# Performance work log

Hardware: AMD Instinct MI355X
Metric: run time of the kernel (lower is better)

The kernel has to match this reference:

```python
import jax, jax.numpy as jnp
import numpy as np

T, B, F, L = 512, 4096, 16, 4  # seq_len, batch, input_size, n_layers; hidden_size H = 1


def _lstm_layer(seq, W_ih, W_hh, b_ih, b_hh):
    """Single unidirectional LSTM layer, H=1.
    seq: [T, B, in]; W_ih: [4, in]; W_hh: [4, 1]; b_ih, b_hh: [4].
    Returns (hs [T,B,1], h_T [B,1], c_T [B,1]). Gate order i,f,g,o (PyTorch).
    """
    # Input contribution for all timesteps at once (the only sizeable GEMM).
    gx = jnp.einsum('tbi,gi->tbg', seq, W_ih) + b_ih + b_hh  # [T, B, 4]
    Bb = seq.shape[1]
    h0 = jnp.zeros((Bb, 1), seq.dtype)
    c0 = jnp.zeros((Bb, 1), seq.dtype)

    def step(carry, g):
        h, c = carry
        gates = g + h @ W_hh.T  # [B, 4]
        i = jax.nn.sigmoid(gates[:, 0:1])
        f = jax.nn.sigmoid(gates[:, 1:2])
        gg = jnp.tanh(gates[:, 2:3])
        o = jax.nn.sigmoid(gates[:, 3:4])
        c = f * c + i * gg
        h = o * jnp.tanh(c)
        return (h, c), h

    (hT, cT), hs = jax.lax.scan(step, (h0, c0), gx)
    return hs, hT, cT


def setup_inputs() -> dict:
    key = jax.random.key(0)
    ks = jax.random.split(key, 6)
    s = 0.5  # ~U(-1,1) stdev scale; 1/sqrt(H)=1 in torch init
    return {
        'x': jax.random.normal(ks[0], (T, B, F), jnp.float32),
        'W_ih0': jax.random.normal(ks[1], (4, F), jnp.float32) * s,
        'W_ih_rest': jax.random.normal(ks[2], (L - 1, 4, 1), jnp.float32) * s,
        'W_hh': jax.random.normal(ks[3], (L, 4, 1), jnp.float32) * s,
        'b_ih': jax.random.normal(ks[4], (L, 4), jnp.float32) * s,
        'b_hh': jax.random.normal(ks[5], (L, 4), jnp.float32) * s,
    }


def reference(x, W_ih0, W_ih_rest, W_hh, b_ih, b_hh):
    seq = x
    hns, cns = [], []
    for l in range(L):
        W_ih_l = W_ih0 if l == 0 else W_ih_rest[l - 1]
        seq, hT, cT = _lstm_layer(seq, W_ih_l, W_hh[l], b_ih[l], b_hh[l])
        hns.append(hT)
        cns.append(cT)
    output = seq                      # [T, B, 1] last-layer hidden sequence
    hn = jnp.stack(hns, axis=0)       # [L, B, 1]
    cn = jnp.stack(cns, axis=0)       # [L, B, 1]
    return output, hn, cn
```

## Files before the change

kernel.cpp:

```cpp
#include <hip/hip_runtime.h>

#define T_DIM 512
#define B_DIM 4096
#define L_DIM 4
#define LOG2E 1.44269504088896f

typedef float f4 __attribute__((ext_vector_type(4)));

template <int CTRL>
__device__ __forceinline__ float dpp_mov(float v) {
  int r = __builtin_amdgcn_update_dpp(0, __builtin_bit_cast(int, v), CTRL, 0xf, 0xf, true);
  return __builtin_bit_cast(float, r);
}
template <int CTRL>
__device__ __forceinline__ float qp_add(float v) { return v + dpp_mov<CTRL>(v); }

__global__ __launch_bounds__(256, 1) void lstm_fused(
    const float* __restrict__ x,
    const float* __restrict__ Wih0,
    const float* __restrict__ Wrest,
    const float* __restrict__ Whh,
    const float* __restrict__ bih, const float* __restrict__ bhh,
    float* __restrict__ out) {
  const int tid = threadIdx.x;
  const int lane = tid & 63;
  const int wid = tid >> 6;
  const int g = lane & 3;
  const int l = (lane >> 2) & 3;
  const int c = (lane >> 4) & 3;
  const int chain = blockIdx.x * 16 + wid * 4 + c;
  const bool l0 = (l == 0);

  auto sg = [](int i) { return (i == 2) ? 2.0f * LOG2E : -LOG2E; };

  const float whh  = sg(g) * Whh[l * 4 + g];
  const float wih  = l0 ? 0.f : sg(g) * Wrest[(l - 1) * 4 + g];
  const float base = l0 ? 0.f : sg(g) * (bih[l * 4 + g] + bhh[l * 4 + g]);
  f4 wx;
  {
    const f4 wv = ((const f4*)Wih0)[g * 4 + l];
    const float s = sg(g);
    wx.x = s * wv.x; wx.y = s * wv.y; wx.z = s * wv.z; wx.w = s * wv.w;
  }
  const float dinit = l0 ? sg(g) * (bih[g] + bhh[g]) : 0.f;
  const float vm = (g == 2) ? -2.f : 1.f;
  const float va = (g == 2) ? 1.f : 0.f;

  const f4* __restrict__ xp = (const f4*)x;
  const size_t xoff = (size_t)chain * 4 + (size_t)l;
  float* __restrict__ po = out + chain;

  float h = 0.f, cs = 0.f;
  f4 A[8], B[8];

#define LOAD8(R, t0)                                                        \
  do {                                                                      \
    R[0] = xp[(size_t)((t0) + 0) * 16384 + xoff];                           \
    R[1] = xp[(size_t)((t0) + 1) * 16384 + xoff];                           \
    R[2] = xp[(size_t)((t0) + 2) * 16384 + xoff];                           \
    R[3] = xp[(size_t)((t0) + 3) * 16384 + xoff];                           \
    R[4] = xp[(size_t)((t0) + 4) * 16384 + xoff];                           \
    R[5] = xp[(size_t)((t0) + 5) * 16384 + xoff];                           \
    R[6] = xp[(size_t)((t0) + 6) * 16384 + xoff];                           \
    R[7] = xp[(size_t)((t0) + 7) * 16384 + xoff];                           \
  } while (0)

  auto dotD = [&](f4 xv) -> float {
    float p = fmaf(xv.x, wx.x, fmaf(xv.y, wx.y, fmaf(xv.z, wx.z, fmaf(xv.w, wx.w, dinit))));
    p = qp_add<0x124>(p);
    p = qp_add<0x128>(p);
    return p;
  };

  auto cellv = [&](int k, float D, bool guard) {
    float hin = dpp_mov<0x114>(h);
    float pb = l0 ? D : base;
    float gate = fmaf(whh, h, fmaf(wih, hin, pb));

    float r = __builtin_amdgcn_rcpf(1.0f + __builtin_amdgcn_exp2f(gate));
    float v = fmaf(vm, r, va);

    float i_ = dpp_mov<0x00>(v);
    float f_ = dpp_mov<0x55>(v);
    float tg = dpp_mov<0xAA>(v);
    float o_ = dpp_mov<0xFF>(v);
    float cn = fmaf(f_, cs, i_ * tg);
    float tcn = fmaf(-2.0f,
        __builtin_amdgcn_rcpf(1.0f + __builtin_amdgcn_exp2f(2.88539008178f * cn)), 1.0f);
    float hm = o_ * tcn;

    if (guard) {
      const bool valid = (unsigned)(k - l) < (unsigned)T_DIM;
      cs = valid ? cn : cs;
      h  = valid ? hm : h;
    } else {
      cs = cn; h = hm;
    }
    const int t = k - 3;
    if (l == 3 && g == 0 && (unsigned)t < (unsigned)T_DIM)
      po[(size_t)t * B_DIM] = hm;
  };

#define CELLS8(R, k0, guard)                                                \
  do {                                                                      \
    float D0_ = dotD(R[0]), D1_ = dotD(R[1]), D2_ = dotD(R[2]),             \
          D3_ = dotD(R[3]), D4_ = dotD(R[4]), D5_ = dotD(R[5]),             \
          D6_ = dotD(R[6]), D7_ = dotD(R[7]);                               \
    cellv((k0) + 0, D0_, guard);                                            \
    cellv((k0) + 1, D1_, guard);                                            \
    cellv((k0) + 2, D2_, guard);                                            \
    cellv((k0) + 3, D3_, guard);                                            \
    cellv((k0) + 4, D4_, guard);                                            \
    cellv((k0) + 5, D5_, guard);                                            \
    cellv((k0) + 6, D6_, guard);                                            \
    cellv((k0) + 7, D7_, guard);                                            \
  } while (0)

  LOAD8(A, 0);
  LOAD8(B, 8);
  CELLS8(A, 0, true);
#pragma unroll 1
  for (int n = 1; n < 63; n += 2) {
    LOAD8(A, 8 * (n + 1));
    CELLS8(B, 8 * n, false);
    LOAD8(B, 8 * (n + 2));
    CELLS8(A, 8 * (n + 1), false);
  }
  CELLS8(B, 504, false);
  CELLS8(B, 512, true);

  if (g == 0) {
    po[(size_t)T_DIM * B_DIM + (size_t)l * B_DIM] = h;
    po[(size_t)T_DIM * B_DIM + (size_t)L_DIM * B_DIM + (size_t)l * B_DIM] = cs;
  }
#undef LOAD8
#undef CELLS8
}

extern "C" void kernel_launch(void* const* d_in, const int* in_sizes, int n_in,
                              void* d_out, int out_size, void* d_ws, size_t ws_size,
                              hipStream_t stream) {
  const float* x     = (const float*)d_in[0];
  const float* Wih0  = (const float*)d_in[1];
  const float* Wrest = (const float*)d_in[2];
  const float* Whh   = (const float*)d_in[3];
  const float* bih   = (const float*)d_in[4];
  const float* bhh   = (const float*)d_in[5];
  float* out = (float*)d_out;
  lstm_fused<<<B_DIM / 16, 256, 0, stream>>>(x, Wih0, Wrest, Whh, bih, bhh, out);
}
```

Before: 219.8 us.

## Load x as scalars per lane with DPP rotation and prescale cell state

```diff
diff --git a/kernel.cpp b/kernel.cpp
--- a/kernel.cpp
+++ b/kernel.cpp
@@ -4,8 +4,8 @@
 #define B_DIM 4096
 #define L_DIM 4
 #define LOG2E 1.44269504088896f
-
-typedef float f4 __attribute__((ext_vector_type(4)));
+#define TWOLOG2E 2.88539008177793f
+#define HALF_LN2 0.346573590279973f
 
 template <int CTRL>
 __device__ __forceinline__ float dpp_mov(float v) {
@@ -36,37 +36,45 @@
   const float whh  = sg(g) * Whh[l * 4 + g];
   const float wih  = l0 ? 0.f : sg(g) * Wrest[(l - 1) * 4 + g];
   const float base = l0 ? 0.f : sg(g) * (bih[l * 4 + g] + bhh[l * 4 + g]);
-  f4 wx;
+
+  float wq0, wq1, wq2, wq3;
   {
-    const f4 wv = ((const f4*)Wih0)[g * 4 + l];
     const float s = sg(g);
-    wx.x = s * wv.x; wx.y = s * wv.y; wx.z = s * wv.z; wx.w = s * wv.w;
+    wq0 = s * Wih0[g * 16 + 4 * l + ((g + 0) & 3)];
+    wq1 = s * Wih0[g * 16 + 4 * l + ((g + 1) & 3)];
+    wq2 = s * Wih0[g * 16 + 4 * l + ((g + 2) & 3)];
+    wq3 = s * Wih0[g * 16 + 4 * l + ((g + 3) & 3)];
   }
   const float dinit = l0 ? sg(g) * (bih[g] + bhh[g]) : 0.f;
-  const float vm = (g == 2) ? -2.f : 1.f;
-  const float va = (g == 2) ? 1.f : 0.f;
+  const float vm = (g == 2) ? -2.f * TWOLOG2E : 1.f;
+  const float va = (g == 2) ? TWOLOG2E : 0.f;
 
-  const f4* __restrict__ xp = (const f4*)x;
-  const size_t xoff = (size_t)chain * 4 + (size_t)l;
+  const float* __restrict__ xp = x + (size_t)chain * 16 + (size_t)(4 * l + g);
   float* __restrict__ po = out + chain;
 
-  float h = 0.f, cs = 0.f;
-  f4 A[8], B[8];
+  float h = 0.f, cse = 0.f;
+  float A[8], B[8];
 
 #define LOAD8(R, t0)                                                        \
   do {                                                                      \
-    R[0] = xp[(size_t)((t0) + 0) * 16384 + xoff];                           \
-    R[1] = xp[(size_t)((t0) + 1) * 16384 + xoff];                           \
-    R[2] = xp[(size_t)((t0) + 2) * 16384 + xoff];                           \
-    R[3] = xp[(size_t)((t0) + 3) * 16384 + xoff];                           \
-    R[4] = xp[(size_t)((t0) + 4) * 16384 + xoff];                           \
-    R[5] = xp[(size_t)((t0) + 5) * 16384 + xoff];                           \
-    R[6] = xp[(size_t)((t0) + 6) * 16384 + xoff];                           \
-    R[7] = xp[(size_t)((t0) + 7) * 16384 + xoff];                           \
+    R[0] = xp[(size_t)((t0) + 0) * 65536];                                  \
+    R[1] = xp[(size_t)((t0) + 1) * 65536];                                  \
+    R[2] = xp[(size_t)((t0) + 2) * 65536];                                  \
+    R[3] = xp[(size_t)((t0) + 3) * 65536];                                  \
+    R[4] = xp[(size_t)((t0) + 4) * 65536];                                  \
+    R[5] = xp[(size_t)((t0) + 5) * 65536];                                  \
+    R[6] = xp[(size_t)((t0) + 6) * 65536];                                  \
+    R[7] = xp[(size_t)((t0) + 7) * 65536];                                  \
   } while (0)
 
-  auto dotD = [&](f4 xv) -> float {
-    float p = fmaf(xv.x, wx.x, fmaf(xv.y, wx.y, fmaf(xv.z, wx.z, fmaf(xv.w, wx.w, dinit))));
+  auto dotD = [&](float xv) -> float {
+    float x1 = dpp_mov<0x39>(xv);
+    float x2 = dpp_mov<0x4E>(xv);
+    float x3 = dpp_mov<0x93>(xv);
+    float p = fmaf(xv, wq0, dinit);
+    p = fmaf(x1, wq1, p);
+    p = fmaf(x2, wq2, p);
+    p = fmaf(x3, wq3, p);
     p = qp_add<0x124>(p);
     p = qp_add<0x128>(p);
     return p;
@@ -80,21 +88,21 @@
     float r = __builtin_amdgcn_rcpf(1.0f + __builtin_amdgcn_exp2f(gate));
     float v = fmaf(vm, r, va);
 
-    float i_ = dpp_mov<0x00>(v);
-    float f_ = dpp_mov<0x55>(v);
-    float tg = dpp_mov<0xAA>(v);
-    float o_ = dpp_mov<0xFF>(v);
-    float cn = fmaf(f_, cs, i_ * tg);
+    float i_  = dpp_mov<0x00>(v);
+    float f_  = dpp_mov<0x55>(v);
+    float tgs = dpp_mov<0xAA>(v);
+    float o_  = dpp_mov<0xFF>(v);
+    float cne = fmaf(f_, cse, i_ * tgs);
     float tcn = fmaf(-2.0f,
-        __builtin_amdgcn_rcpf(1.0f + __builtin_amdgcn_exp2f(2.88539008178f * cn)), 1.0f);
+        __builtin_amdgcn_rcpf(1.0f + __builtin_amdgcn_exp2f(cne)), 1.0f);
     float hm = o_ * tcn;
 
     if (guard) {
       const bool valid = (unsigned)(k - l) < (unsigned)T_DIM;
-      cs = valid ? cn : cs;
-      h  = valid ? hm : h;
+      cse = valid ? cne : cse;
+      h   = valid ? hm : h;
     } else {
-      cs = cn; h = hm;
+      cse = cne; h = hm;
     }
     const int t = k - 3;
     if (l == 3 && g == 0 && (unsigned)t < (unsigned)T_DIM)
@@ -131,7 +139,8 @@
 
   if (g == 0) {
     po[(size_t)T_DIM * B_DIM + (size_t)l * B_DIM] = h;
-    po[(size_t)T_DIM * B_DIM + (size_t)L_DIM * B_DIM + (size_t)l * B_DIM] = cs;
+    po[(size_t)T_DIM * B_DIM + (size_t)L_DIM * B_DIM + (size_t)l * B_DIM] =
+        cse * HALF_LN2;
   }
 #undef LOAD8
 #undef CELLS8
```

Measured after the change: 218.3 us. About the same (-0.7%).
